# Kernel optimization log

Measured on AMD Instinct MI355X. Metric: run time of the kernel, lower is better.

Reference implementation:

```python
import jax, jax.numpy as jnp
import numpy as np


def setup_inputs() -> dict:
    key = jax.random.key(0)
    k1, k2 = jax.random.split(key)
    B, Lq, Ls, D = 16, 2048, 2048, 512
    query = jax.random.normal(k1, (B, Lq, D), dtype=jnp.float32)
    support = jax.random.normal(k2, (B, Ls, D), dtype=jnp.float32)
    return {"query": query, "support": support}


def reference(query, support):
    # attn: [B, Lq, Ls] = softmax(query @ support^T, axis=-1)
    logits = jnp.einsum("bqd,bsd->bqs", query, support)
    attn = jax.nn.softmax(logits, axis=-1)
    # attended support: [B, Lq, D]
    attended = jnp.einsum("bqs,bsd->bqd", attn, support)
    # score: [B, Lq] = sum over D of query * attended
    score = jnp.sum(query * attended, axis=-1)
    return score
```

## Files before the change

### kernel.cpp

```cpp
#include <hip/hip_runtime.h>
#include <hip/hip_bf16.h>

#define B_  16
#define LQ  2048
#define LS  2048
#define DD  512
#define BQ  128
#define BS  128
#define BK  64
#define NSB (LS / BS)
#define NKC (DD / BK)
#define NSPLIT 4

typedef short bf16x8 __attribute__((ext_vector_type(8)));
typedef float f32x4  __attribute__((ext_vector_type(4)));

__device__ __forceinline__ void load_lds16(const void* g, void* l) {
  __builtin_amdgcn_global_load_lds((const __attribute__((address_space(1))) void*)g,
                                   (__attribute__((address_space(3))) void*)l,
                                   16, 0, 0);
}

__device__ __forceinline__ unsigned short f2bf(float f) {
  union { float f; unsigned int u; } v; v.f = f;
  unsigned int r = v.u + 0x7fffu + ((v.u >> 16) & 1u);
  return (unsigned short)(r >> 16);
}

__global__ __launch_bounds__(256) void cvt_kernel(const float* __restrict__ Q,
                                                  const float* __restrict__ S,
                                                  unsigned short* __restrict__ Qw,
                                                  unsigned short* __restrict__ Sw,
                                                  int nblk) {
  int blk = blockIdx.x;
  const float* src; unsigned short* dst;
  if (blk < nblk) { src = Q; dst = Qw; } else { src = S; dst = Sw; blk -= nblk; }
  int i = blk * 256 + threadIdx.x;
  float4 f = ((const float4*)src)[i];
  ushort4 u;
  u.x = f2bf(f.x); u.y = f2bf(f.y); u.z = f2bf(f.z); u.w = f2bf(f.w);
  ((ushort4*)dst)[i] = u;
}

__global__ __launch_bounds__(512, 4) void attn_kernel(const unsigned short* __restrict__ Qw,
                                                      const unsigned short* __restrict__ Sw,
                                                      float* __restrict__ out,
                                                      float* __restrict__ pm,
                                                      float* __restrict__ pse,
                                                      float* __restrict__ psel,
                                                      int nsplit) {
  __shared__ __align__(16) unsigned short sQ[BQ * BK];
  __shared__ __align__(16) unsigned short sS[BS * BK];

  const int qb   = blockIdx.x;
  const int b    = blockIdx.y;
  const int spl  = blockIdx.z;
  const int tid  = threadIdx.x;
  const int w    = tid >> 6;
  const int lane = tid & 63;
  const int h    = w & 1;
  const int g    = w >> 1;
  const int col  = lane & 15;
  const int quad = lane >> 4;
  const int c7   = col & 7;

  const int q0 = qb * BQ;
  const unsigned short* Qb = Qw + (size_t)b * LQ * DD;
  const unsigned short* Sb = Sw + (size_t)b * LS * DD;

  float mst[2] = { -INFINITY, -INFINITY };
  float se[2]  = { 0.f, 0.f };
  float sel[2] = { 0.f, 0.f };

  f32x4 acc[4][2];

  const int rr    = lane >> 3;
  const int cc    = ((lane & 7) ^ rr) * 8;
  const int srow0 = (w & 3) * 32;

  const int sbs = spl * (NSB / nsplit);
  const int sbe = sbs + (NSB / nsplit);

  for (int sb = sbs; sb < sbe; ++sb) {
    const int s0 = sb * BS;
#pragma unroll
    for (int st = 0; st < 4; ++st)
#pragma unroll
      for (int qt = 0; qt < 2; ++qt)
        acc[st][qt] = (f32x4){0.f, 0.f, 0.f, 0.f};

    for (int kc = 0; kc < NKC; ++kc) {
      __syncthreads();
      if (w < 4) {
#pragma unroll
        for (int i = 0; i < 4; ++i) {
          int r = srow0 + i * 8 + rr;
          load_lds16(Qb + (size_t)(q0 + r) * DD + kc * BK + cc, &sQ[(srow0 + i * 8) * BK]);
        }
      } else {
#pragma unroll
        for (int i = 0; i < 4; ++i) {
          int r = srow0 + i * 8 + rr;
          load_lds16(Sb + (size_t)(s0 + r) * DD + kc * BK + cc, &sS[(srow0 + i * 8) * BK]);
        }
      }
      __syncthreads();

#pragma unroll
      for (int kk = 0; kk < 2; ++kk) {
        const int koff = ((kk * 4 + quad) ^ c7) * 8;
        bf16x8 aq[2], asv[4];
#pragma unroll
        for (int qt = 0; qt < 2; ++qt)
          aq[qt] = *(const bf16x8*)&sQ[(g * 32 + qt * 16 + col) * BK + koff];
#pragma unroll
        for (int st = 0; st < 4; ++st)
          asv[st] = *(const bf16x8*)&sS[(h * 64 + st * 16 + col) * BK + koff];
#pragma unroll
        for (int st = 0; st < 4; ++st)
#pragma unroll
          for (int qt = 0; qt < 2; ++qt)
            acc[st][qt] = __builtin_amdgcn_mfma_f32_16x16x32_bf16(asv[st], aq[qt], acc[st][qt], 0, 0, 0);
      }
    }

#pragma unroll
    for (int qt = 0; qt < 2; ++qt) {
      float lmax = mst[qt];
#pragma unroll
      for (int st = 0; st < 4; ++st)
#pragma unroll
        for (int r = 0; r < 4; ++r)
          lmax = fmaxf(lmax, acc[st][qt][r]);
      lmax = fmaxf(lmax, __shfl_xor(lmax, 16, 64));
      lmax = fmaxf(lmax, __shfl_xor(lmax, 32, 64));
      float alpha = __expf(mst[qt] - lmax);
      float pe = 0.f, pel = 0.f;
#pragma unroll
      for (int st = 0; st < 4; ++st)
#pragma unroll
        for (int r = 0; r < 4; ++r) {
          float l = acc[st][qt][r];
          float e = __expf(l - lmax);
          pe += e;
          pel = fmaf(e, l, pel);
        }
      pe  += __shfl_xor(pe, 16, 64);  pe  += __shfl_xor(pe, 32, 64);
      pel += __shfl_xor(pel, 16, 64); pel += __shfl_xor(pel, 32, 64);
      se[qt]  = fmaf(se[qt],  alpha, pe);
      sel[qt] = fmaf(sel[qt], alpha, pel);
      mst[qt] = lmax;
    }
  }

  __syncthreads();
  float* red = (float*)sQ;
  if (quad == 0) {
#pragma unroll
    for (int qt = 0; qt < 2; ++qt) {
      int idx = ((g * 2 + h) * 2 + qt) * 16 + col;
      red[idx]       = mst[qt];
      red[256 + idx] = se[qt];
      red[512 + idx] = sel[qt];
    }
  }
  __syncthreads();
  if (h == 0 && quad == 0) {
#pragma unroll
    for (int qt = 0; qt < 2; ++qt) {
      int i0 = ((g * 2 + 0) * 2 + qt) * 16 + col;
      int i1 = ((g * 2 + 1) * 2 + qt) * 16 + col;
      float m0 = red[i0], m1 = red[i1];
      float M  = fmaxf(m0, m1);
      float a0 = __expf(m0 - M), a1 = __expf(m1 - M);
      float SE  = red[256 + i0] * a0 + red[256 + i1] * a1;
      float SEL = red[512 + i0] * a0 + red[512 + i1] * a1;
      size_t qi = (size_t)b * LQ + q0 + g * 32 + qt * 16 + col;
      if (nsplit == 1) {
        out[qi] = SEL / SE;
      } else {
        pm[qi * NSPLIT + spl]   = M;
        pse[qi * NSPLIT + spl]  = SE;
        psel[qi * NSPLIT + spl] = SEL;
      }
    }
  }
}

__global__ __launch_bounds__(256) void combine_kernel(const float* __restrict__ pm,
                                                      const float* __restrict__ pse,
                                                      const float* __restrict__ psel,
                                                      float* __restrict__ out) {
  int i = blockIdx.x * blockDim.x + threadIdx.x;
  if (i >= B_ * LQ) return;
  float M = -INFINITY;
#pragma unroll
  for (int s = 0; s < NSPLIT; ++s) M = fmaxf(M, pm[i * NSPLIT + s]);
  float SE = 0.f, SEL = 0.f;
#pragma unroll
  for (int s = 0; s < NSPLIT; ++s) {
    float a = __expf(pm[i * NSPLIT + s] - M);
    SE  = fmaf(pse[i * NSPLIT + s],  a, SE);
    SEL = fmaf(psel[i * NSPLIT + s], a, SEL);
  }
  out[i] = SEL / SE;
}

__global__ __launch_bounds__(256) void fallback_kernel(const float* __restrict__ Q,
                                                       const float* __restrict__ S,
                                                       float* __restrict__ out) {
  __shared__ float qv[DD];
  __shared__ float red[256];
  const int b = blockIdx.y, qi = blockIdx.x, tid = threadIdx.x;
  const float* qrow = Q + ((size_t)b * LQ + qi) * DD;
  for (int d = tid; d < DD; d += 256) qv[d] = qrow[d];
  __syncthreads();
  const float* Sb = S + (size_t)b * LS * DD;
  float m = -INFINITY, se = 0.f, sel = 0.f;
  for (int s = tid; s < LS; s += 256) {
    const float* srow = Sb + (size_t)s * DD;
    float dot = 0.f;
    for (int d = 0; d < DD; ++d) dot = fmaf(qv[d], srow[d], dot);
    float mn = fmaxf(m, dot);
    float a = __expf(m - mn);
    float e = __expf(dot - mn);
    se  = se * a + e;
    sel = sel * a + e * dot;
    m = mn;
  }
  red[tid] = m; __syncthreads();
  for (int o = 128; o > 0; o >>= 1) { if (tid < o) red[tid] = fmaxf(red[tid], red[tid + o]); __syncthreads(); }
  float M = red[0]; __syncthreads();
  float a = __expf(m - M); se *= a; sel *= a;
  red[tid] = se; __syncthreads();
  for (int o = 128; o > 0; o >>= 1) { if (tid < o) red[tid] += red[tid + o]; __syncthreads(); }
  float SE = red[0]; __syncthreads();
  red[tid] = sel; __syncthreads();
  for (int o = 128; o > 0; o >>= 1) { if (tid < o) red[tid] += red[tid + o]; __syncthreads(); }
  float SEL = red[0];
  if (tid == 0) out[(size_t)b * LQ + qi] = SEL / SE;
}

extern "C" void kernel_launch(void* const* d_in, const int* in_sizes, int n_in,
                              void* d_out, int out_size, void* d_ws, size_t ws_size,
                              hipStream_t stream) {
  const float* Q = (const float*)d_in[0];
  const float* S = (const float*)d_in[1];
  float* out = (float*)d_out;
  const size_t nelem = (size_t)B_ * LQ * DD;
  const size_t need_base  = 2 * nelem * sizeof(unsigned short);
  const size_t part_elems = (size_t)B_ * LQ * NSPLIT;
  const size_t need_split = need_base + 3 * part_elems * sizeof(float);

  if (ws_size >= need_base) {
    unsigned short* Qw = (unsigned short*)d_ws;
    unsigned short* Sw = Qw + nelem;
    int nblk = (int)(nelem / 4 / 256);
    cvt_kernel<<<2 * nblk, 256, 0, stream>>>(Q, S, Qw, Sw, nblk);
    if (ws_size >= need_split) {
      float* pm   = (float*)(Sw + nelem);
      float* pse  = pm + part_elems;
      float* psel = pse + part_elems;
      attn_kernel<<<dim3(LQ / BQ, B_, NSPLIT), 512, 0, stream>>>(Qw, Sw, out, pm, pse, psel, NSPLIT);
      combine_kernel<<<(B_ * LQ + 255) / 256, 256, 0, stream>>>(pm, pse, psel, out);
    } else {
      attn_kernel<<<dim3(LQ / BQ, B_, 1), 512, 0, stream>>>(Qw, Sw, out, nullptr, nullptr, nullptr, 1);
    }
  } else {
    fallback_kernel<<<dim3(LQ, B_), 256, 0, stream>>>(Q, S, out);
  }
}
```

Baseline: 231.8 us.

## Double-buffer LDS tiles with async prefetch and remap block IDs for locality

```diff
diff --git a/kernel.cpp b/kernel.cpp
--- a/kernel.cpp
+++ b/kernel.cpp
@@ -11,6 +11,8 @@
 #define NSB (LS / BS)
 #define NKC (DD / BK)
 #define NSPLIT 4
+
+static_assert(NKC == 8, "stage>>3 math assumes NKC==8");
 
 typedef short bf16x8 __attribute__((ext_vector_type(8)));
 typedef float f32x4  __attribute__((ext_vector_type(4)));
@@ -49,12 +51,16 @@
                                                       float* __restrict__ pse,
                                                       float* __restrict__ psel,
                                                       int nsplit) {
-  __shared__ __align__(16) unsigned short sQ[BQ * BK];
-  __shared__ __align__(16) unsigned short sS[BS * BK];
-
-  const int qb   = blockIdx.x;
-  const int b    = blockIdx.y;
-  const int spl  = blockIdx.z;
+  __shared__ __align__(16) unsigned short sQ[2][BQ * BK];
+  __shared__ __align__(16) unsigned short sS[2][BS * BK];
+
+  const int pid = blockIdx.x + (blockIdx.y << 4) + (blockIdx.z << 8);
+  const int nch = (nsplit << 8) >> 3;
+  const int lid = (pid & 7) * nch + (pid >> 3);
+  const int qb  = lid & 15;
+  const int b   = (lid >> 4) & 15;
+  const int spl = lid >> 8;
+
   const int tid  = threadIdx.x;
   const int w    = tid >> 6;
   const int lane = tid & 63;
@@ -73,88 +79,114 @@
   float sel[2] = { 0.f, 0.f };
 
   f32x4 acc[4][2];
+#pragma unroll
+  for (int st = 0; st < 4; ++st)
+#pragma unroll
+    for (int qt = 0; qt < 2; ++qt)
+      acc[st][qt] = (f32x4){0.f, 0.f, 0.f, 0.f};
 
   const int rr    = lane >> 3;
   const int cc    = ((lane & 7) ^ rr) * 8;
   const int srow0 = (w & 3) * 32;
 
   const int sbs = spl * (NSB / nsplit);
-  const int sbe = sbs + (NSB / nsplit);
-
-  for (int sb = sbs; sb < sbe; ++sb) {
-    const int s0 = sb * BS;
-#pragma unroll
-    for (int st = 0; st < 4; ++st)
+  const int nst = (NSB / nsplit) * NKC;
+
+  auto issue_stage = [&](int sb_i, int kc_i, int buf) {
+    if (w < 4) {
+#pragma unroll
+      for (int i = 0; i < 4; ++i) {
+        int r0 = srow0 + i * 8;
+        load_lds16(Qb + (size_t)(q0 + r0 + rr) * DD + kc_i * BK + cc, &sQ[buf][r0 * BK]);
+      }
+    } else {
+      const int s0i = sb_i * BS;
+#pragma unroll
+      for (int i = 0; i < 4; ++i) {
+        int r0 = srow0 + i * 8;
+        load_lds16(Sb + (size_t)(s0i + r0 + rr) * DD + kc_i * BK + cc, &sS[buf][r0 * BK]);
+      }
+    }
+  };
+
+  issue_stage(sbs, 0, 0);
+  int cur = 0;
+
+#pragma unroll 1
+  for (int t = 0; t < nst; ++t) {
+    asm volatile("s_waitcnt lgkmcnt(0)" ::: "memory");
+    __builtin_amdgcn_s_barrier();
+
+    const int tn = t + 1;
+    if (tn < nst) {
+      issue_stage(sbs + (tn >> 3), tn & 7, cur ^ 1);
+      asm volatile("s_waitcnt vmcnt(4)" ::: "memory");
+    } else {
+      asm volatile("s_waitcnt vmcnt(0)" ::: "memory");
+    }
+    __builtin_amdgcn_s_barrier();
+    __builtin_amdgcn_sched_barrier(0);
+
+    const unsigned short* bq = &sQ[cur][0];
+    const unsigned short* bs = &sS[cur][0];
+    __builtin_amdgcn_s_setprio(1);
+#pragma unroll
+    for (int kk = 0; kk < 2; ++kk) {
+      const int koff = ((kk * 4 + quad) ^ c7) * 8;
+      bf16x8 aq[2], asv[4];
 #pragma unroll
       for (int qt = 0; qt < 2; ++qt)
-        acc[st][qt] = (f32x4){0.f, 0.f, 0.f, 0.f};
-
-    for (int kc = 0; kc < NKC; ++kc) {
-      __syncthreads();
-      if (w < 4) {
-#pragma unroll
-        for (int i = 0; i < 4; ++i) {
-          int r = srow0 + i * 8 + rr;
-          load_lds16(Qb + (size_t)(q0 + r) * DD + kc * BK + cc, &sQ[(srow0 + i * 8) * BK]);
-        }
-      } else {
-#pragma unroll
-        for (int i = 0; i < 4; ++i) {
-          int r = srow0 + i * 8 + rr;
-          load_lds16(Sb + (size_t)(s0 + r) * DD + kc * BK + cc, &sS[(srow0 + i * 8) * BK]);
-        }
+        aq[qt] = *(const bf16x8*)&bq[(g * 32 + qt * 16 + col) * BK + koff];
+#pragma unroll
+      for (int st = 0; st < 4; ++st)
+        asv[st] = *(const bf16x8*)&bs[(h * 64 + st * 16 + col) * BK + koff];
+#pragma unroll
+      for (int st = 0; st < 4; ++st)
+#pragma unroll
+        for (int qt = 0; qt < 2; ++qt)
+          acc[st][qt] = __builtin_amdgcn_mfma_f32_16x16x32_bf16(asv[st], aq[qt], acc[st][qt], 0, 0, 0);
+    }
+    __builtin_amdgcn_s_setprio(0);
+    cur ^= 1;
+
+    if ((t & (NKC - 1)) == NKC - 1) {
+#pragma unroll
+      for (int qt = 0; qt < 2; ++qt) {
+        float lmax = mst[qt];
+#pragma unroll
+        for (int st = 0; st < 4; ++st)
+#pragma unroll
+          for (int r = 0; r < 4; ++r)
+            lmax = fmaxf(lmax, acc[st][qt][r]);
+        lmax = fmaxf(lmax, __shfl_xor(lmax, 16, 64));
+        lmax = fmaxf(lmax, __shfl_xor(lmax, 32, 64));
+        float alpha = __expf(mst[qt] - lmax);
+        float pe = 0.f, pel = 0.f;
+#pragma unroll
+        for (int st = 0; st < 4; ++st)
+#pragma unroll
+          for (int r = 0; r < 4; ++r) {
+            float l = acc[st][qt][r];
+            float e = __expf(l - lmax);
+            pe += e;
+            pel = fmaf(e, l, pel);
+          }
+        pe  += __shfl_xor(pe, 16, 64);  pe  += __shfl_xor(pe, 32, 64);
+        pel += __shfl_xor(pel, 16, 64); pel += __shfl_xor(pel, 32, 64);
+        se[qt]  = fmaf(se[qt],  alpha, pe);
+        sel[qt] = fmaf(sel[qt], alpha, pel);
+        mst[qt] = lmax;
       }
-      __syncthreads();
-
-#pragma unroll
-      for (int kk = 0; kk < 2; ++kk) {
-        const int koff = ((kk * 4 + quad) ^ c7) * 8;
-        bf16x8 aq[2], asv[4];
+#pragma unroll
+      for (int st = 0; st < 4; ++st)
 #pragma unroll
         for (int qt = 0; qt < 2; ++qt)
-          aq[qt] = *(const bf16x8*)&sQ[(g * 32 + qt * 16 + col) * BK + koff];
-#pragma unroll
-        for (int st = 0; st < 4; ++st)
-          asv[st] = *(const bf16x8*)&sS[(h * 64 + st * 16 + col) * BK + koff];
-#pragma unroll
-        for (int st = 0; st < 4; ++st)
-#pragma unroll
-          for (int qt = 0; qt < 2; ++qt)
-            acc[st][qt] = __builtin_amdgcn_mfma_f32_16x16x32_bf16(asv[st], aq[qt], acc[st][qt], 0, 0, 0);
-      }
-    }
-
-#pragma unroll
-    for (int qt = 0; qt < 2; ++qt) {
-      float lmax = mst[qt];
-#pragma unroll
-      for (int st = 0; st < 4; ++st)
-#pragma unroll
-        for (int r = 0; r < 4; ++r)
-          lmax = fmaxf(lmax, acc[st][qt][r]);
-      lmax = fmaxf(lmax, __shfl_xor(lmax, 16, 64));
-      lmax = fmaxf(lmax, __shfl_xor(lmax, 32, 64));
-      float alpha = __expf(mst[qt] - lmax);
-      float pe = 0.f, pel = 0.f;
-#pragma unroll
-      for (int st = 0; st < 4; ++st)
-#pragma unroll
-        for (int r = 0; r < 4; ++r) {
-          float l = acc[st][qt][r];
-          float e = __expf(l - lmax);
-          pe += e;
-          pel = fmaf(e, l, pel);
-        }
-      pe  += __shfl_xor(pe, 16, 64);  pe  += __shfl_xor(pe, 32, 64);
-      pel += __shfl_xor(pel, 16, 64); pel += __shfl_xor(pel, 32, 64);
-      se[qt]  = fmaf(se[qt],  alpha, pe);
-      sel[qt] = fmaf(sel[qt], alpha, pel);
-      mst[qt] = lmax;
+          acc[st][qt] = (f32x4){0.f, 0.f, 0.f, 0.f};
     }
   }
 
   __syncthreads();
-  float* red = (float*)sQ;
+  float* red = (float*)&sQ[0][0];
   if (quad == 0) {
 #pragma unroll
     for (int qt = 0; qt < 2; ++qt) {
```

Result: no change. 234.8 us (+1.3%).
